# Kernel optimization log

Measured on AMD Instinct MI355X. Metric: run time of the kernel, lower is better.

## Reference

```python
import jax, jax.numpy as jnp
import numpy as np

N = 100000   # nodes
E = 1600000  # edges
DIN, DH, DOUT = 128, 64, 40
EPS = 1e-5


def setup_inputs() -> dict:
    key = jax.random.key(0)
    ks = jax.random.split(key, 16)
    glorot = lambda k, shp: jax.random.normal(k, shp, jnp.float32) / np.float32(np.sqrt(shp[0]))
    return {
        'x': jax.random.normal(ks[0], (N, DIN), jnp.float32),
        'edge_index': jax.random.randint(ks[1], (2, E), 0, N, jnp.int64),
        'W0': glorot(ks[2], (DIN, DH)), 'b0': jnp.zeros((DH,), jnp.float32),
        'W1': glorot(ks[3], (DH, DH)),  'b1': jnp.zeros((DH,), jnp.float32),
        'W2': glorot(ks[4], (DH, DH)),  'b2': jnp.zeros((DH,), jnp.float32),
        'ln0_g': jnp.ones((DH,), jnp.float32), 'ln0_b': jnp.zeros((DH,), jnp.float32),
        'ln1_g': jnp.ones((DH,), jnp.float32), 'ln1_b': jnp.zeros((DH,), jnp.float32),
        'mpW0': glorot(ks[5], (DH, DH)),  'mpb0': jnp.zeros((DH,), jnp.float32),
        'mpW1': glorot(ks[6], (DH, DOUT)), 'mpb1': jnp.zeros((DOUT,), jnp.float32),
    }


def _layernorm(h, g, b):
    mu = jnp.mean(h, axis=-1, keepdims=True)
    var = jnp.mean(jnp.square(h - mu), axis=-1, keepdims=True)
    return (h - mu) * jax.lax.rsqrt(var + EPS) * g + b


def _gcn_conv(x, src, dst, norm_e, self_w, W, b):
    # PyG GCNConv: h = x W; out = sum_{(s,d)} norm * h[s] scattered to d,
    # plus self-loop term, plus bias.  norm = d^{-1/2}[s] * d^{-1/2}[d] on A+I.
    h = x @ W                                        # [N, out]
    agg = jnp.zeros_like(h).at[dst].add(h[src] * norm_e[:, None])
    agg = agg + h * self_w[:, None]                  # self loops (i,i)
    return agg + b


def reference(x, edge_index, W0, b0, W1, b1, W2, b2,
              ln0_g, ln0_b, ln1_g, ln1_b, mpW0, mpb0, mpW1, mpb1):
    src, dst = edge_index[0], edge_index[1]
    # degree on A + I (count incoming edges at dst, +1 for self loop)
    deg = jnp.zeros((N,), jnp.float32).at[dst].add(1.0) + 1.0
    dinv = jax.lax.rsqrt(deg)
    norm_e = dinv[src] * dinv[dst]                   # per-edge weight [E]
    self_w = dinv * dinv                             # self-loop weight [N]

    h = x
    convs = [(W0, b0), (W1, b1), (W2, b2)]
    lns = [(ln0_g, ln0_b), (ln1_g, ln1_b)]
    for i, (W, b) in enumerate(convs):
        h = _gcn_conv(h, src, dst, norm_e, self_w, W, b)
        h = jax.nn.relu(h)
        # dropout: training=False -> identity
        if i != len(convs) - 1:
            g, bb = lns[i]
            h = _layernorm(h, g, bb)

    # post_mp: Linear -> Dropout(identity) -> Linear
    h = h @ mpW0 + mpb0
    return h @ mpW1 + mpb1
```

## Files before the change

### kernel.cpp

```cpp
#include <hip/hip_runtime.h>
#include <hip/hip_bf16.h>

#define NN 100000
#define EE 1600000
#define DOUT 40
#define LN_EPS 1e-5f
#define NBUCK 391
#define TILE 4096
#define TBLK 391
#define BCAP 8192

typedef __attribute__((ext_vector_type(8))) short short8;
typedef __attribute__((ext_vector_type(4))) float f32x4;

__device__ __forceinline__ float blo(unsigned u) { return __uint_as_float(u << 16); }
__device__ __forceinline__ float bhi(unsigned u) { return __uint_as_float(u & 0xffff0000u); }
__device__ __forceinline__ unsigned bpack(float lo, float hi) {
    unsigned a = __float_as_uint(lo);
    unsigned b = __float_as_uint(hi);
    a = (a + 0x7fffu + ((a >> 16) & 1u)) >> 16;
    b = (b + 0x7fffu + ((b >> 16) & 1u)) & 0xffff0000u;
    return (a & 0xffffu) | b;
}

__global__ __launch_bounds__(512, 8) void bucket_k(const int* __restrict__ src,
                                                   const int* __restrict__ dst,
                                                   int* __restrict__ bucketCur,
                                                   unsigned* __restrict__ bE) {
    __shared__ int cnt[8][NBUCK];
    __shared__ int basew[8][NBUCK];
    int tid = threadIdx.x;
    int wv = tid >> 6;
    for (int i = tid; i < 8 * NBUCK; i += 512) ((int*)cnt)[i] = 0;
    __syncthreads();
    long e0 = (long)blockIdx.x * TILE;
    int d[8];
#pragma unroll
    for (int i = 0; i < 8; ++i) {
        long e = e0 + tid + i * 512;
        d[i] = (e < EE) ? dst[e] : -1;
    }
#pragma unroll
    for (int i = 0; i < 8; ++i) {
        if (d[i] >= 0) atomicAdd(&cnt[wv][d[i] >> 8], 1);
    }
    __syncthreads();
    for (int b = tid; b < NBUCK; b += 512) {
        int c[8];
        int tot = 0;
#pragma unroll
        for (int w = 0; w < 8; ++w) { c[w] = cnt[w][b]; tot += c[w]; }
        int base = tot ? atomicAdd(&bucketCur[b], tot) : 0;
        int run = b * BCAP + base;
#pragma unroll
        for (int w = 0; w < 8; ++w) { basew[w][b] = run; run += c[w]; cnt[w][b] = 0; }
    }
    __syncthreads();
#pragma unroll
    for (int i = 0; i < 8; ++i) {
        if (d[i] >= 0) {
            long e = e0 + tid + i * 512;
            int b = d[i] >> 8;
            int pos = basew[wv][b] + atomicAdd(&cnt[wv][b], 1);
            bE[pos] = (unsigned)src[e] | ((unsigned)(d[i] & 255) << 24);
        }
    }
}

__global__ __launch_bounds__(512, 4) void reorder2_k(const int* __restrict__ bucketCur,
                                                     const unsigned* __restrict__ bE,
                                                     int* __restrict__ csrSrc,
                                                     int* __restrict__ degI,
                                                     int* __restrict__ cursor,
                                                     float* __restrict__ dinv) {
    __shared__ int sScan[512];
    __shared__ int sHist[256];
    __shared__ int sPre[256];
    __shared__ int sStart[256];
    int tid = threadIdx.x;
    int b = blockIdx.x;
    int c = (tid < NBUCK) ? bucketCur[tid] : 0;
    sScan[tid] = c;
    __syncthreads();
    for (int off = 1; off < 512; off <<= 1) {
        int t = (tid >= off) ? sScan[tid - off] : 0;
        __syncthreads();
        sScan[tid] += t;
        __syncthreads();
    }
    int bbase = (b == 0) ? 0 : sScan[b - 1];
    if (tid < 256) sHist[tid] = 0;
    __syncthreads();
    int start = b * BCAP;
    int end = start + bucketCur[b];
    for (int e = start + tid; e < end; e += 512) {
        unsigned v = bE[e];
        atomicAdd(&sHist[v >> 24], 1);
    }
    __syncthreads();
    if (tid < 256) sPre[tid] = sHist[tid];
    __syncthreads();
    for (int off = 1; off < 256; off <<= 1) {
        int t = (tid >= off && tid < 256) ? sPre[tid - off] : 0;
        __syncthreads();
        if (tid < 256) sPre[tid] += t;
        __syncthreads();
    }
    if (tid < 256) {
        int h = sHist[tid];
        int excl = sPre[tid] - h;
        int st = bbase + excl;
        sStart[tid] = st;
        int nd = (b << 8) + tid;
        if (nd < NN) {
            degI[nd] = h;
            cursor[nd] = st;
            dinv[nd] = rsqrtf((float)h + 1.0f);
        }
    }
    __syncthreads();
    for (int e = start + tid; e < end; e += 512) {
        unsigned v = bE[e];
        int pos = atomicAdd(&sStart[v >> 24], 1);
        csrSrc[pos] = (int)(v & 0xFFFFFFu);
    }
}

__global__ void prep_k(const float* __restrict__ W0, const float* __restrict__ W1,
                       const float* __restrict__ W2,
                       const float* __restrict__ mpW0, const float* __restrict__ mpb0,
                       const float* __restrict__ mpW1, const float* __restrict__ mpb1,
                       uint4* __restrict__ W0pk, uint4* __restrict__ W1pk,
                       uint4* __restrict__ W2pk, uint4* __restrict__ Wfpk,
                       float* __restrict__ bf) {
    __shared__ float sWf[64 * 48];
    int tid = threadIdx.x;
    for (int i = tid; i < 64 * 48; i += 256) {
        int k = i / 48, n = i % 48;
        float acc = 0.f;
        if (n < DOUT) {
            for (int j = 0; j < 64; ++j) acc = fmaf(mpW0[k * 64 + j], mpW1[j * DOUT + n], acc);
        }
        sWf[i] = acc;
    }
    for (int n = tid; n < 48; n += 256) {
        float acc = 0.f;
        if (n < DOUT) {
            acc = mpb1[n];
            for (int j = 0; j < 64; ++j) acc = fmaf(mpb0[j], mpW1[j * DOUT + n], acc);
        }
        bf[n] = acc;
    }
    for (int i = tid; i < 1024; i += 256) {
        int lane = i & 63, ct = i >> 6;
        int q = lane >> 4, ln = lane & 15;
        int c = ct >> 2, t = ct & 3;
        int row0 = c * 32 + q * 8, col = t * 16 + ln;
        uint4 u;
        u.x = bpack(W0[(row0 + 0) * 64 + col], W0[(row0 + 1) * 64 + col]);
        u.y = bpack(W0[(row0 + 2) * 64 + col], W0[(row0 + 3) * 64 + col]);
        u.z = bpack(W0[(row0 + 4) * 64 + col], W0[(row0 + 5) * 64 + col]);
        u.w = bpack(W0[(row0 + 6) * 64 + col], W0[(row0 + 7) * 64 + col]);
        W0pk[i] = u;
    }
    for (int i = tid; i < 512; i += 256) {
        int lane = i & 63, ct = i >> 6;
        int q = lane >> 4, ln = lane & 15;
        int c = ct >> 2, t = ct & 3;
        int row0 = c * 32 + q * 8, col = t * 16 + ln;
        uint4 u;
        u.x = bpack(W1[(row0 + 0) * 64 + col], W1[(row0 + 1) * 64 + col]);
        u.y = bpack(W1[(row0 + 2) * 64 + col], W1[(row0 + 3) * 64 + col]);
        u.z = bpack(W1[(row0 + 4) * 64 + col], W1[(row0 + 5) * 64 + col]);
        u.w = bpack(W1[(row0 + 6) * 64 + col], W1[(row0 + 7) * 64 + col]);
        W1pk[i] = u;
        uint4 v;
        v.x = bpack(W2[(row0 + 0) * 64 + col], W2[(row0 + 1) * 64 + col]);
        v.y = bpack(W2[(row0 + 2) * 64 + col], W2[(row0 + 3) * 64 + col]);
        v.z = bpack(W2[(row0 + 4) * 64 + col], W2[(row0 + 5) * 64 + col]);
        v.w = bpack(W2[(row0 + 6) * 64 + col], W2[(row0 + 7) * 64 + col]);
        W2pk[i] = v;
    }
    __syncthreads();
    for (int i = tid; i < 384; i += 256) {
        int lane = i & 63, ct = i >> 6;
        int q = lane >> 4, ln = lane & 15;
        int c = ct / 3, t = ct % 3;
        int row0 = c * 32 + q * 8, col = t * 16 + ln;
        uint4 u;
        u.x = bpack(sWf[(row0 + 0) * 48 + col], sWf[(row0 + 1) * 48 + col]);
        u.y = bpack(sWf[(row0 + 2) * 48 + col], sWf[(row0 + 3) * 48 + col]);
        u.z = bpack(sWf[(row0 + 4) * 48 + col], sWf[(row0 + 5) * 48 + col]);
        u.w = bpack(sWf[(row0 + 6) * 48 + col], sWf[(row0 + 7) * 48 + col]);
        Wfpk[i] = u;
    }
}

__global__ __launch_bounds__(256, 2) void gemm0(const float* __restrict__ X,
                                                const uint4* __restrict__ Wpk,
                                                const float* __restrict__ dinv,
                                                unsigned* __restrict__ H) {
    __shared__ float sD[64 * 65];
    int tid = threadIdx.x;
    int wv = tid >> 6, lane = tid & 63;
    int q = lane >> 4, ln = lane & 15;
    short8 bfrag[4][4];
#pragma unroll
    for (int c = 0; c < 4; ++c)
#pragma unroll
        for (int t = 0; t < 4; ++t)
            bfrag[c][t] = __builtin_bit_cast(short8, Wpk[(c * 4 + t) * 64 + lane]);
    int base = blockIdx.x * 64;
    int node = base + wv * 16 + ln;
    bool ok = node < NN;
    short8 afrag[4];
#pragma unroll
    for (int c = 0; c < 4; ++c) {
        float4 f0 = make_float4(0.f, 0.f, 0.f, 0.f);
        float4 f1 = make_float4(0.f, 0.f, 0.f, 0.f);
        if (ok) {
            const float4* xp = (const float4*)(X + (long)node * 128 + c * 32 + q * 8);
            f0 = xp[0];
            f1 = xp[1];
        }
        uint4 u;
        u.x = bpack(f0.x, f0.y);
        u.y = bpack(f0.z, f0.w);
        u.z = bpack(f1.x, f1.y);
        u.w = bpack(f1.z, f1.w);
        afrag[c] = __builtin_bit_cast(short8, u);
    }
#pragma unroll
    for (int t = 0; t < 4; ++t) {
        f32x4 acc = {0.f, 0.f, 0.f, 0.f};
#pragma unroll
        for (int c = 0; c < 4; ++c)
            acc = __builtin_amdgcn_mfma_f32_16x16x32_bf16(afrag[c], bfrag[c][t], acc, 0, 0, 0);
#pragma unroll
        for (int r = 0; r < 4; ++r)
            sD[(wv * 16 + q * 4 + r) * 65 + t * 16 + ln] = acc[r];
    }
    __syncthreads();
    for (int i = tid; i < 64 * 32; i += 256) {
        int row = i >> 5, c2 = i & 31;
        int nd = base + row;
        if (nd < NN) {
            float di = dinv[nd];
            float lo = sD[row * 65 + c2 * 2] * di;
            float hi = sD[row * 65 + c2 * 2 + 1] * di;
            H[nd * 32 + c2] = bpack(lo, hi);
        }
    }
}

__global__ __launch_bounds__(256, 2) void gemm_b(const uint4* __restrict__ Hin4,
                                                 const uint4* __restrict__ Wpk,
                                                 const float* __restrict__ dinv,
                                                 unsigned* __restrict__ H) {
    __shared__ float sD[64 * 65];
    int tid = threadIdx.x;
    int wv = tid >> 6, lane = tid & 63;
    int q = lane >> 4, ln = lane & 15;
    short8 bfrag[2][4];
#pragma unroll
    for (int c = 0; c < 2; ++c)
#pragma unroll
        for (int t = 0; t < 4; ++t)
            bfrag[c][t] = __builtin_bit_cast(short8, Wpk[(c * 4 + t) * 64 + lane]);
    int base = blockIdx.x * 64;
    int node = base + wv * 16 + ln;
    bool ok = node < NN;
    short8 afrag[2];
    {
        uint4 u0 = make_uint4(0u, 0u, 0u, 0u), u1 = u0;
        if (ok) {
            u0 = Hin4[(unsigned)node * 8u + (unsigned)q];
            u1 = Hin4[(unsigned)node * 8u + 4u + (unsigned)q];
        }
        afrag[0] = __builtin_bit_cast(short8, u0);
        afrag[1] = __builtin_bit_cast(short8, u1);
    }
#pragma unroll
    for (int t = 0; t < 4; ++t) {
        f32x4 acc = {0.f, 0.f, 0.f, 0.f};
        acc = __builtin_amdgcn_mfma_f32_16x16x32_bf16(afrag[0], bfrag[0][t], acc, 0, 0, 0);
        acc = __builtin_amdgcn_mfma_f32_16x16x32_bf16(afrag[1], bfrag[1][t], acc, 0, 0, 0);
#pragma unroll
        for (int r = 0; r < 4; ++r)
            sD[(wv * 16 + q * 4 + r) * 65 + t * 16 + ln] = acc[r];
    }
    __syncthreads();
    for (int i = tid; i < 64 * 32; i += 256) {
        int row = i >> 5, c2 = i & 31;
        int nd = base + row;
        if (nd < NN) {
            float di = dinv[nd];
            float lo = sD[row * 65 + c2 * 2] * di;
            float hi = sD[row * 65 + c2 * 2 + 1] * di;
            H[nd * 32 + c2] = bpack(lo, hi);
        }
    }
}

__global__ __launch_bounds__(256, 4) void agg_k(
        const int* __restrict__ cursor, const int* __restrict__ degI,
        const int* __restrict__ csrSrc, const float* __restrict__ dinv,
        const uint2* __restrict__ H2, const float4* __restrict__ bias4,
        const float4* __restrict__ g4, const float4* __restrict__ beta4,
        uint2* __restrict__ OUT2, int doLN) {
    int tid = threadIdx.x;
    int w = tid >> 6, lane = tid & 63;
    int g = lane >> 4;
    unsigned f = (unsigned)(lane & 15);
    unsigned node = (unsigned)(blockIdx.x * 4 + w);
    int start = cursor[node];
    int deg = degI[node];
    int myIdx = 0;
    if (lane < deg) myIdx = csrSrc[(unsigned)(start + lane)];
    uint2 qs = H2[node * 16u + f];
    float di = dinv[node];
    float4 bb = bias4[f];
    float ax = 0.f, ay = 0.f, az = 0.f, aw = 0.f;
    float bx = 0.f, by = 0.f, bz = 0.f, bw = 0.f;
    uint2 qa[4];
#pragma unroll
    for (int r = 0; r < 4; ++r) {
        int e = r * 4 + g;
        unsigned s = (unsigned)__shfl(myIdx, e);
        qa[r] = make_uint2(0u, 0u);
        if (e < deg) qa[r] = H2[s * 16u + f];
    }
    if (deg <= 16) {
#pragma unroll
        for (int r = 0; r < 4; r += 2) {
            ax += blo(qa[r].x);     ay += bhi(qa[r].x);
            az += blo(qa[r].y);     aw += bhi(qa[r].y);
            bx += blo(qa[r + 1].x); by += bhi(qa[r + 1].x);
            bz += blo(qa[r + 1].y); bw += bhi(qa[r + 1].y);
        }
    } else {
        uint2 qb[4];
#pragma unroll
        for (int r = 0; r < 4; ++r) {
            int e = 16 + r * 4 + g;
            unsigned s = (unsigned)__shfl(myIdx, e);
            qb[r] = make_uint2(0u, 0u);
            if (e < deg) qb[r] = H2[s * 16u + f];
        }
#pragma unroll
        for (int r = 0; r < 4; r += 2) {
            ax += blo(qa[r].x);     ay += bhi(qa[r].x);
            az += blo(qa[r].y);     aw += bhi(qa[r].y);
            bx += blo(qa[r + 1].x); by += bhi(qa[r + 1].x);
            bz += blo(qa[r + 1].y); bw += bhi(qa[r + 1].y);
        }
#pragma unroll
        for (int r = 0; r < 4; r += 2) {
            ax += blo(qb[r].x);     ay += bhi(qb[r].x);
            az += blo(qb[r].y);     aw += bhi(qb[r].y);
            bx += blo(qb[r + 1].x); by += bhi(qb[r + 1].x);
            bz += blo(qb[r + 1].y); bw += bhi(qb[r + 1].y);
        }
        if (deg > 32) {
            int R2 = (deg + 3) >> 2;
            if (R2 > 16) R2 = 16;
            for (int r = 8; r < R2; ++r) {
                int e = r * 4 + g;
                unsigned s = (unsigned)__shfl(myIdx, e);
                uint2 qq = make_uint2(0u, 0u);
                if (e < deg) qq = H2[s * 16u + f];
                ax += blo(qq.x); ay += bhi(qq.x); az += blo(qq.y); aw += bhi(qq.y);
            }
            for (int ee = 64 + g; ee < deg; ee += 4) {
                uint2 qq = H2[(unsigned)csrSrc[(unsigned)(start + ee)] * 16u + f];
                ax += blo(qq.x); ay += bhi(qq.x); az += blo(qq.y); aw += bhi(qq.y);
            }
        }
    }
    ax += bx; ay += by; az += bz; aw += bw;
    ax += __shfl_xor(ax, 16); ay += __shfl_xor(ay, 16);
    az += __shfl_xor(az, 16); aw += __shfl_xor(aw, 16);
    ax += __shfl_xor(ax, 32); ay += __shfl_xor(ay, 32);
    az += __shfl_xor(az, 32); aw += __shfl_xor(aw, 32);
    float vx = fmaxf((ax + blo(qs.x)) * di + bb.x, 0.f);
    float vy = fmaxf((ay + bhi(qs.x)) * di + bb.y, 0.f);
    float vz = fmaxf((az + blo(qs.y)) * di + bb.z, 0.f);
    float vw = fmaxf((aw + bhi(qs.y)) * di + bb.w, 0.f);
    if (doLN) {
        float s = vx + vy + vz + vw;
        s += __shfl_xor(s, 1); s += __shfl_xor(s, 2);
        s += __shfl_xor(s, 4); s += __shfl_xor(s, 8);
        float mu = s * (1.f / 64.f);
        vx -= mu; vy -= mu; vz -= mu; vw -= mu;
        float vs = vx * vx + vy * vy + vz * vz + vw * vw;
        vs += __shfl_xor(vs, 1); vs += __shfl_xor(vs, 2);
        vs += __shfl_xor(vs, 4); vs += __shfl_xor(vs, 8);
        float inv = rsqrtf(vs * (1.f / 64.f) + LN_EPS);
        float4 gg = g4[f];
        float4 tt = beta4[f];
        vx = vx * inv * gg.x + tt.x;
        vy = vy * inv * gg.y + tt.y;
        vz = vz * inv * gg.z + tt.z;
        vw = vw * inv * gg.w + tt.w;
    }
    if (g == 0) OUT2[node * 16u + f] = make_uint2(bpack(vx, vy), bpack(vz, vw));
}

__global__ __launch_bounds__(256, 2) void mlp_mfma(const uint4* __restrict__ Hin4,
                                                   const uint4* __restrict__ Wfpk,
                                                   const float* __restrict__ bf,
                                                   float* __restrict__ OUT) {
    int tid = threadIdx.x;
    int wv = tid >> 6, lane = tid & 63;
    int q = lane >> 4, ln = lane & 15;
    short8 bfrag[2][3];
#pragma unroll
    for (int c = 0; c < 2; ++c)
#pragma unroll
        for (int t = 0; t < 3; ++t)
            bfrag[c][t] = __builtin_bit_cast(short8, Wfpk[(c * 3 + t) * 64 + lane]);
    int base = blockIdx.x * 64;
    int node = base + wv * 16 + ln;
    bool ok = node < NN;
    short8 afrag[2];
    {
        uint4 u0 = make_uint4(0u, 0u, 0u, 0u), u1 = u0;
        if (ok) {
            u0 = Hin4[(unsigned)node * 8u + (unsigned)q];
            u1 = Hin4[(unsigned)node * 8u + 4u + (unsigned)q];
        }
        afrag[0] = __builtin_bit_cast(short8, u0);
        afrag[1] = __builtin_bit_cast(short8, u1);
    }
#pragma unroll
    for (int t = 0; t < 3; ++t) {
        f32x4 acc = {0.f, 0.f, 0.f, 0.f};
        acc = __builtin_amdgcn_mfma_f32_16x16x32_bf16(afrag[0], bfrag[0][t], acc, 0, 0, 0);
        acc = __builtin_amdgcn_mfma_f32_16x16x32_bf16(afrag[1], bfrag[1][t], acc, 0, 0, 0);
        int col = t * 16 + ln;
        if (col < DOUT) {
            float bv = bf[col];
#pragma unroll
            for (int r = 0; r < 4; ++r) {
                int nd = base + wv * 16 + q * 4 + r;
                if (nd < NN) OUT[(long)nd * DOUT + col] = acc[r] + bv;
            }
        }
    }
}

extern "C" void kernel_launch(void* const* d_in, const int* in_sizes, int n_in,
                              void* d_out, int out_size, void* d_ws, size_t ws_size,
                              hipStream_t stream) {
    const float* x    = (const float*)d_in[0];
    const int*   ei   = (const int*)d_in[1];
    const int*   srcI = ei;
    const int*   dstI = ei + EE;
    const float* W0   = (const float*)d_in[2];
    const float* b0   = (const float*)d_in[3];
    const float* W1   = (const float*)d_in[4];
    const float* b1   = (const float*)d_in[5];
    const float* W2   = (const float*)d_in[6];
    const float* b2   = (const float*)d_in[7];
    const float* ln0g = (const float*)d_in[8];
    const float* ln0b = (const float*)d_in[9];
    const float* ln1g = (const float*)d_in[10];
    const float* ln1b = (const float*)d_in[11];
    const float* mpW0 = (const float*)d_in[12];
    const float* mpb0 = (const float*)d_in[13];
    const float* mpW1 = (const float*)d_in[14];
    const float* mpb1 = (const float*)d_in[15];
    float* out = (float*)d_out;

    char* ws = (char*)d_ws;
    float*    dinv      = (float*)   (ws + 0);
    int*      degI      = (int*)     (ws + 512l * 1024);
    int*      cursor    = (int*)     (ws + 1024l * 1024);
    int*      bucketCur = (int*)     (ws + 1600l * 1024);
    uint4*    W0pk      = (uint4*)   (ws + 1792l * 1024);
    uint4*    W1pk      = (uint4*)   (ws + 1824l * 1024);
    uint4*    W2pk      = (uint4*)   (ws + 1856l * 1024);
    uint4*    Wfpk      = (uint4*)   (ws + 1888l * 1024);
    float*    bfv       = (float*)   (ws + 1920l * 1024);
    unsigned* bE        = (unsigned*)(ws + 2048l * 1024);
    int*      csrSrc    = (int*)     (ws + 15l * 1024 * 1024);
    unsigned* bufA      = (unsigned*)(ws + 22l * 1024 * 1024);
    unsigned* bufB      = (unsigned*)(ws + 36l * 1024 * 1024);

    const int aggBlocks  = NN / 4;
    const int gemmBlocks = (NN + 63) / 64;

    hipMemsetAsync(bucketCur, 0, NBUCK * sizeof(int), stream);
    bucket_k<<<TBLK, 512, 0, stream>>>(srcI, dstI, bucketCur, bE);
    reorder2_k<<<NBUCK, 512, 0, stream>>>(bucketCur, bE, csrSrc, degI, cursor, dinv);
    prep_k<<<1, 256, 0, stream>>>(W0, W1, W2, mpW0, mpb0, mpW1, mpb1,
                                  W0pk, W1pk, W2pk, Wfpk, bfv);

    gemm0<<<gemmBlocks, 256, 0, stream>>>(x, W0pk, dinv, bufA);
    agg_k<<<aggBlocks, 256, 0, stream>>>(cursor, degI, csrSrc, dinv, (const uint2*)bufA,
                                         (const float4*)b0, (const float4*)ln0g,
                                         (const float4*)ln0b, (uint2*)bufB, 1);
    gemm_b<<<gemmBlocks, 256, 0, stream>>>((const uint4*)bufB, W1pk, dinv, bufA);
    agg_k<<<aggBlocks, 256, 0, stream>>>(cursor, degI, csrSrc, dinv, (const uint2*)bufA,
                                         (const float4*)b1, (const float4*)ln1g,
                                         (const float4*)ln1b, (uint2*)bufB, 1);
    gemm_b<<<gemmBlocks, 256, 0, stream>>>((const uint4*)bufB, W2pk, dinv, bufA);
    agg_k<<<aggBlocks, 256, 0, stream>>>(cursor, degI, csrSrc, dinv, (const uint2*)bufA,
                                         (const float4*)b2, (const float4*)ln0g,
                                         (const float4*)ln0b, (uint2*)bufB, 0);
    mlp_mfma<<<gemmBlocks, 256, 0, stream>>>((const uint4*)bufB, Wfpk, bfv, out);
}
```

Baseline: 328.3 us.

## Fold weight prep into bucket kernel, vectorize edge loads, reload B fragments per MFMA

Drops the single-block prep_k launch by running the weight packing in one extra block of bucket_k. Edge src/dst reads in bucket_k and bucket entry reads in reorder2_k move to 128-bit vector loads. The GEMM and MLP kernels now load B fragments from global memory inside the MFMA loop rather than preloading them into registers, and their occupancy hint rises from 2 to 4 blocks. The aim is to cut launch overhead and register pressure, at the cost of repeated small weight loads that should mostly hit cache.

```diff
diff --git a/kernel.cpp b/kernel.cpp
--- a/kernel.cpp
+++ b/kernel.cpp
@@ -23,22 +23,97 @@
     return (a & 0xffffu) | b;
 }
 
-__global__ __launch_bounds__(512, 8) void bucket_k(const int* __restrict__ src,
-                                                   const int* __restrict__ dst,
-                                                   int* __restrict__ bucketCur,
-                                                   unsigned* __restrict__ bE) {
+__global__ __launch_bounds__(512, 4) void bucket_k(
+        const int* __restrict__ src, const int* __restrict__ dst,
+        int* __restrict__ bucketCur, unsigned* __restrict__ bE,
+        const float* __restrict__ W0, const float* __restrict__ W1,
+        const float* __restrict__ W2,
+        const float* __restrict__ mpW0, const float* __restrict__ mpb0,
+        const float* __restrict__ mpW1, const float* __restrict__ mpb1,
+        uint4* __restrict__ W0pk, uint4* __restrict__ W1pk,
+        uint4* __restrict__ W2pk, uint4* __restrict__ Wfpk,
+        float* __restrict__ bf) {
     __shared__ int cnt[8][NBUCK];
     __shared__ int basew[8][NBUCK];
+    __shared__ float sWf[64 * 48];
     int tid = threadIdx.x;
+    if (blockIdx.x == TBLK) {
+        for (int i = tid; i < 64 * 48; i += 512) {
+            int k = i / 48, n = i % 48;
+            float acc = 0.f;
+            if (n < DOUT) {
+                for (int j = 0; j < 64; ++j) acc = fmaf(mpW0[k * 64 + j], mpW1[j * DOUT + n], acc);
+            }
+            sWf[i] = acc;
+        }
+        for (int n = tid; n < 48; n += 512) {
+            float acc = 0.f;
+            if (n < DOUT) {
+                acc = mpb1[n];
+                for (int j = 0; j < 64; ++j) acc = fmaf(mpb0[j], mpW1[j * DOUT + n], acc);
+            }
+            bf[n] = acc;
+        }
+        for (int i = tid; i < 1024; i += 512) {
+            int lane = i & 63, ct = i >> 6;
+            int q = lane >> 4, ln = lane & 15;
+            int c = ct >> 2, t = ct & 3;
+            int row0 = c * 32 + q * 8, col = t * 16 + ln;
+            uint4 u;
+            u.x = bpack(W0[(row0 + 0) * 64 + col], W0[(row0 + 1) * 64 + col]);
+            u.y = bpack(W0[(row0 + 2) * 64 + col], W0[(row0 + 3) * 64 + col]);
+            u.z = bpack(W0[(row0 + 4) * 64 + col], W0[(row0 + 5) * 64 + col]);
+            u.w = bpack(W0[(row0 + 6) * 64 + col], W0[(row0 + 7) * 64 + col]);
+            W0pk[i] = u;
+        }
+        for (int i = tid; i < 512; i += 512) {
+            int lane = i & 63, ct = i >> 6;
+            int q = lane >> 4, ln = lane & 15;
+            int c = ct >> 2, t = ct & 3;
+            int row0 = c * 32 + q * 8, col = t * 16 + ln;
+            uint4 u;
+            u.x = bpack(W1[(row0 + 0) * 64 + col], W1[(row0 + 1) * 64 + col]);
+            u.y = bpack(W1[(row0 + 2) * 64 + col], W1[(row0 + 3) * 64 + col]);
+            u.z = bpack(W1[(row0 + 4) * 64 + col], W1[(row0 + 5) * 64 + col]);
+            u.w = bpack(W1[(row0 + 6) * 64 + col], W1[(row0 + 7) * 64 + col]);
+            W1pk[i] = u;
+            uint4 v;
+            v.x = bpack(W2[(row0 + 0) * 64 + col], W2[(row0 + 1) * 64 + col]);
+            v.y = bpack(W2[(row0 + 2) * 64 + col], W2[(row0 + 3) * 64 + col]);
+            v.z = bpack(W2[(row0 + 4) * 64 + col], W2[(row0 + 5) * 64 + col]);
+            v.w = bpack(W2[(row0 + 6) * 64 + col], W2[(row0 + 7) * 64 + col]);
+            W2pk[i] = v;
+        }
+        __syncthreads();
+        for (int i = tid; i < 384; i += 512) {
+            int lane = i & 63, ct = i >> 6;
+            int q = lane >> 4, ln = lane & 15;
+            int c = ct / 3, t = ct % 3;
+            int row0 = c * 32 + q * 8, col = t * 16 + ln;
+            uint4 u;
+            u.x = bpack(sWf[(row0 + 0) * 48 + col], sWf[(row0 + 1) * 48 + col]);
+            u.y = bpack(sWf[(row0 + 2) * 48 + col], sWf[(row0 + 3) * 48 + col]);
+            u.z = bpack(sWf[(row0 + 4) * 48 + col], sWf[(row0 + 5) * 48 + col]);
+            u.w = bpack(sWf[(row0 + 6) * 48 + col], sWf[(row0 + 7) * 48 + col]);
+            Wfpk[i] = u;
+        }
+        return;
+    }
     int wv = tid >> 6;
     for (int i = tid; i < 8 * NBUCK; i += 512) ((int*)cnt)[i] = 0;
     __syncthreads();
-    long e0 = (long)blockIdx.x * TILE;
-    int d[8];
-#pragma unroll
-    for (int i = 0; i < 8; ++i) {
-        long e = e0 + tid + i * 512;
-        d[i] = (e < EE) ? dst[e] : -1;
+    const int4* dst4 = (const int4*)dst;
+    const int4* src4 = (const int4*)src;
+    long base4 = (long)blockIdx.x * (TILE / 4);
+    int d[8], s[8];
+#pragma unroll
+    for (int j = 0; j < 2; ++j) {
+        long i4 = base4 + j * 512 + tid;
+        int4 dv = make_int4(-1, -1, -1, -1);
+        int4 sv = make_int4(0, 0, 0, 0);
+        if (i4 < EE / 4) { dv = dst4[i4]; sv = src4[i4]; }
+        d[j * 4 + 0] = dv.x; d[j * 4 + 1] = dv.y; d[j * 4 + 2] = dv.z; d[j * 4 + 3] = dv.w;
+        s[j * 4 + 0] = sv.x; s[j * 4 + 1] = sv.y; s[j * 4 + 2] = sv.z; s[j * 4 + 3] = sv.w;
     }
 #pragma unroll
     for (int i = 0; i < 8; ++i) {
@@ -59,10 +134,9 @@
 #pragma unroll
     for (int i = 0; i < 8; ++i) {
         if (d[i] >= 0) {
-            long e = e0 + tid + i * 512;
             int b = d[i] >> 8;
             int pos = basew[wv][b] + atomicAdd(&cnt[wv][b], 1);
-            bE[pos] = (unsigned)src[e] | ((unsigned)(d[i] & 255) << 24);
+            bE[pos] = (unsigned)s[i] | ((unsigned)(d[i] & 255) << 24);
         }
     }
 }
@@ -92,10 +166,18 @@
     if (tid < 256) sHist[tid] = 0;
     __syncthreads();
     int start = b * BCAP;
-    int end = start + bucketCur[b];
-    for (int e = start + tid; e < end; e += 512) {
-        unsigned v = bE[e];
-        atomicAdd(&sHist[v >> 24], 1);
+    int ecnt = bucketCur[b];
+    int nq = ecnt >> 2;
+    const uint4* bE4 = (const uint4*)(bE + start);
+    for (int i = tid; i < nq; i += 512) {
+        uint4 v = bE4[i];
+        atomicAdd(&sHist[v.x >> 24], 1);
+        atomicAdd(&sHist[v.y >> 24], 1);
+        atomicAdd(&sHist[v.z >> 24], 1);
+        atomicAdd(&sHist[v.w >> 24], 1);
+    }
+    for (int e = (nq << 2) + tid; e < ecnt; e += 512) {
+        atomicAdd(&sHist[bE[start + e] >> 24], 1);
     }
     __syncthreads();
     if (tid < 256) sPre[tid] = sHist[tid];
@@ -119,84 +201,25 @@
         }
     }
     __syncthreads();
-    for (int e = start + tid; e < end; e += 512) {
-        unsigned v = bE[e];
+    for (int i = tid; i < nq; i += 512) {
+        uint4 v = bE4[i];
+        int p0 = atomicAdd(&sStart[v.x >> 24], 1);
+        csrSrc[p0] = (int)(v.x & 0xFFFFFFu);
+        int p1 = atomicAdd(&sStart[v.y >> 24], 1);
+        csrSrc[p1] = (int)(v.y & 0xFFFFFFu);
+        int p2 = atomicAdd(&sStart[v.z >> 24], 1);
+        csrSrc[p2] = (int)(v.z & 0xFFFFFFu);
+        int p3 = atomicAdd(&sStart[v.w >> 24], 1);
+        csrSrc[p3] = (int)(v.w & 0xFFFFFFu);
+    }
+    for (int e = (nq << 2) + tid; e < ecnt; e += 512) {
+        unsigned v = bE[start + e];
         int pos = atomicAdd(&sStart[v >> 24], 1);
         csrSrc[pos] = (int)(v & 0xFFFFFFu);
     }
 }
 
-__global__ void prep_k(const float* __restrict__ W0, const float* __restrict__ W1,
-                       const float* __restrict__ W2,
-                       const float* __restrict__ mpW0, const float* __restrict__ mpb0,
-                       const float* __restrict__ mpW1, const float* __restrict__ mpb1,
-                       uint4* __restrict__ W0pk, uint4* __restrict__ W1pk,
-                       uint4* __restrict__ W2pk, uint4* __restrict__ Wfpk,
-                       float* __restrict__ bf) {
-    __shared__ float sWf[64 * 48];
-    int tid = threadIdx.x;
-    for (int i = tid; i < 64 * 48; i += 256) {
-        int k = i / 48, n = i % 48;
-        float acc = 0.f;
-        if (n < DOUT) {
-            for (int j = 0; j < 64; ++j) acc = fmaf(mpW0[k * 64 + j], mpW1[j * DOUT + n], acc);
-        }
-        sWf[i] = acc;
-    }
-    for (int n = tid; n < 48; n += 256) {
-        float acc = 0.f;
-        if (n < DOUT) {
-            acc = mpb1[n];
-            for (int j = 0; j < 64; ++j) acc = fmaf(mpb0[j], mpW1[j * DOUT + n], acc);
-        }
-        bf[n] = acc;
-    }
-    for (int i = tid; i < 1024; i += 256) {
-        int lane = i & 63, ct = i >> 6;
-        int q = lane >> 4, ln = lane & 15;
-        int c = ct >> 2, t = ct & 3;
-        int row0 = c * 32 + q * 8, col = t * 16 + ln;
-        uint4 u;
-        u.x = bpack(W0[(row0 + 0) * 64 + col], W0[(row0 + 1) * 64 + col]);
-        u.y = bpack(W0[(row0 + 2) * 64 + col], W0[(row0 + 3) * 64 + col]);
-        u.z = bpack(W0[(row0 + 4) * 64 + col], W0[(row0 + 5) * 64 + col]);
-        u.w = bpack(W0[(row0 + 6) * 64 + col], W0[(row0 + 7) * 64 + col]);
-        W0pk[i] = u;
-    }
-    for (int i = tid; i < 512; i += 256) {
-        int lane = i & 63, ct = i >> 6;
-        int q = lane >> 4, ln = lane & 15;
-        int c = ct >> 2, t = ct & 3;
-        int row0 = c * 32 + q * 8, col = t * 16 + ln;
-        uint4 u;
-        u.x = bpack(W1[(row0 + 0) * 64 + col], W1[(row0 + 1) * 64 + col]);
-        u.y = bpack(W1[(row0 + 2) * 64 + col], W1[(row0 + 3) * 64 + col]);
-        u.z = bpack(W1[(row0 + 4) * 64 + col], W1[(row0 + 5) * 64 + col]);
-        u.w = bpack(W1[(row0 + 6) * 64 + col], W1[(row0 + 7) * 64 + col]);
-        W1pk[i] = u;
-        uint4 v;
-        v.x = bpack(W2[(row0 + 0) * 64 + col], W2[(row0 + 1) * 64 + col]);
-        v.y = bpack(W2[(row0 + 2) * 64 + col], W2[(row0 + 3) * 64 + col]);
-        v.z = bpack(W2[(row0 + 4) * 64 + col], W2[(row0 + 5) * 64 + col]);
-        v.w = bpack(W2[(row0 + 6) * 64 + col], W2[(row0 + 7) * 64 + col]);
-        W2pk[i] = v;
-    }
-    __syncthreads();
-    for (int i = tid; i < 384; i += 256) {
-        int lane = i & 63, ct = i >> 6;
-        int q = lane >> 4, ln = lane & 15;
-        int c = ct / 3, t = ct % 3;
-        int row0 = c * 32 + q * 8, col = t * 16 + ln;
-        uint4 u;
-        u.x = bpack(sWf[(row0 + 0) * 48 + col], sWf[(row0 + 1) * 48 + col]);
-        u.y = bpack(sWf[(row0 + 2) * 48 + col], sWf[(row0 + 3) * 48 + col]);
-        u.z = bpack(sWf[(row0 + 4) * 48 + col], sWf[(row0 + 5) * 48 + col]);
-        u.w = bpack(sWf[(row0 + 6) * 48 + col], sWf[(row0 + 7) * 48 + col]);
-        Wfpk[i] = u;
-    }
-}
-
-__global__ __launch_bounds__(256, 2) void gemm0(const float* __restrict__ X,
+__global__ __launch_bounds__(256, 4) void gemm0(const float* __restrict__ X,
                                                 const uint4* __restrict__ Wpk,
                                                 const float* __restrict__ dinv,
                                                 unsigned* __restrict__ H) {
@@ -204,12 +227,6 @@
     int tid = threadIdx.x;
     int wv = tid >> 6, lane = tid & 63;
     int q = lane >> 4, ln = lane & 15;
-    short8 bfrag[4][4];
-#pragma unroll
-    for (int c = 0; c < 4; ++c)
-#pragma unroll
-        for (int t = 0; t < 4; ++t)
-            bfrag[c][t] = __builtin_bit_cast(short8, Wpk[(c * 4 + t) * 64 + lane]);
     int base = blockIdx.x * 64;
     int node = base + wv * 16 + ln;
     bool ok = node < NN;
@@ -234,8 +251,10 @@
     for (int t = 0; t < 4; ++t) {
         f32x4 acc = {0.f, 0.f, 0.f, 0.f};
 #pragma unroll
-        for (int c = 0; c < 4; ++c)
-            acc = __builtin_amdgcn_mfma_f32_16x16x32_bf16(afrag[c], bfrag[c][t], acc, 0, 0, 0);
+        for (int c = 0; c < 4; ++c) {
+            short8 bfrag = __builtin_bit_cast(short8, Wpk[(c * 4 + t) * 64 + lane]);
+            acc = __builtin_amdgcn_mfma_f32_16x16x32_bf16(afrag[c], bfrag, acc, 0, 0, 0);
+        }
 #pragma unroll
         for (int r = 0; r < 4; ++r)
             sD[(wv * 16 + q * 4 + r) * 65 + t * 16 + ln] = acc[r];
@@ -253,7 +272,7 @@
     }
 }
 
-__global__ __launch_bounds__(256, 2) void gemm_b(const uint4* __restrict__ Hin4,
+__global__ __launch_bounds__(256, 4) void gemm_b(const uint4* __restrict__ Hin4,
                                                  const uint4* __restrict__ Wpk,
                                                  const float* __restrict__ dinv,
                                                  unsigned* __restrict__ H) {
@@ -261,12 +280,6 @@
     int tid = threadIdx.x;
     int wv = tid >> 6, lane = tid & 63;
     int q = lane >> 4, ln = lane & 15;
-    short8 bfrag[2][4];
-#pragma unroll
-    for (int c = 0; c < 2; ++c)
-#pragma unroll
-        for (int t = 0; t < 4; ++t)
-            bfrag[c][t] = __builtin_bit_cast(short8, Wpk[(c * 4 + t) * 64 + lane]);
     int base = blockIdx.x * 64;
     int node = base + wv * 16 + ln;
     bool ok = node < NN;
@@ -283,8 +296,11 @@
 #pragma unroll
     for (int t = 0; t < 4; ++t) {
         f32x4 acc = {0.f, 0.f, 0.f, 0.f};
-        acc = __builtin_amdgcn_mfma_f32_16x16x32_bf16(afrag[0], bfrag[0][t], acc, 0, 0, 0);
-        acc = __builtin_amdgcn_mfma_f32_16x16x32_bf16(afrag[1], bfrag[1][t], acc, 0, 0, 0);
+#pragma unroll
+        for (int c = 0; c < 2; ++c) {
+            short8 bfrag = __builtin_bit_cast(short8, Wpk[(c * 4 + t) * 64 + lane]);
+            acc = __builtin_amdgcn_mfma_f32_16x16x32_bf16(afrag[c], bfrag, acc, 0, 0, 0);
+        }
 #pragma unroll
         for (int r = 0; r < 4; ++r)
             sD[(wv * 16 + q * 4 + r) * 65 + t * 16 + ln] = acc[r];
@@ -406,19 +422,13 @@
     if (g == 0) OUT2[node * 16u + f] = make_uint2(bpack(vx, vy), bpack(vz, vw));
 }
 
-__global__ __launch_bounds__(256, 2) void mlp_mfma(const uint4* __restrict__ Hin4,
+__global__ __launch_bounds__(256, 4) void mlp_mfma(const uint4* __restrict__ Hin4,
                                                    const uint4* __restrict__ Wfpk,
                                                    const float* __restrict__ bf,
                                                    float* __restrict__ OUT) {
     int tid = threadIdx.x;
     int wv = tid >> 6, lane = tid & 63;
     int q = lane >> 4, ln = lane & 15;
-    short8 bfrag[2][3];
-#pragma unroll
-    for (int c = 0; c < 2; ++c)
-#pragma unroll
-        for (int t = 0; t < 3; ++t)
-            bfrag[c][t] = __builtin_bit_cast(short8, Wfpk[(c * 3 + t) * 64 + lane]);
     int base = blockIdx.x * 64;
     int node = base + wv * 16 + ln;
     bool ok = node < NN;
@@ -435,8 +445,11 @@
 #pragma unroll
     for (int t = 0; t < 3; ++t) {
         f32x4 acc = {0.f, 0.f, 0.f, 0.f};
-        acc = __builtin_amdgcn_mfma_f32_16x16x32_bf16(afrag[0], bfrag[0][t], acc, 0, 0, 0);
-        acc = __builtin_amdgcn_mfma_f32_16x16x32_bf16(afrag[1], bfrag[1][t], acc, 0, 0, 0);
+#pragma unroll
+        for (int c = 0; c < 2; ++c) {
+            short8 bfrag = __builtin_bit_cast(short8, Wfpk[(c * 3 + t) * 64 + lane]);
+            acc = __builtin_amdgcn_mfma_f32_16x16x32_bf16(afrag[c], bfrag, acc, 0, 0, 0);
+        }
         int col = t * 16 + ln;
         if (col < DOUT) {
             float bv = bf[col];
@@ -491,10 +504,10 @@
     const int gemmBlocks = (NN + 63) / 64;
 
     hipMemsetAsync(bucketCur, 0, NBUCK * sizeof(int), stream);
-    bucket_k<<<TBLK, 512, 0, stream>>>(srcI, dstI, bucketCur, bE);
+    bucket_k<<<TBLK + 1, 512, 0, stream>>>(srcI, dstI, bucketCur, bE,
+                                           W0, W1, W2, mpW0, mpb0, mpW1, mpb1,
+                                           W0pk, W1pk, W2pk, Wfpk, bfv);
     reorder2_k<<<NBUCK, 512, 0, stream>>>(bucketCur, bE, csrSrc, degI, cursor, dinv);
-    prep_k<<<1, 256, 0, stream>>>(W0, W1, W2, mpW0, mpb0, mpW1, mpb1,
-                                  W0pk, W1pk, W2pk, Wfpk, bfv);
 
     gemm0<<<gemmBlocks, 256, 0, stream>>>(x, W0pk, dinv, bufA);
     agg_k<<<aggBlocks, 256, 0, stream>>>(cursor, degI, csrSrc, dinv, (const uint2*)bufA,
```

After: 312.3 us. 1.05x faster.
